# Performance work log

Hardware: AMD Instinct MI355X
Metric: run time of the kernel (lower is better)

Reference implementation:

```python
import jax, jax.numpy as jnp
import numpy as np

I = 256   # input_size
H = 256   # hidden_size
B = 64
T = 2048


def setup_inputs() -> dict:
    key = jax.random.key(0)
    ks = jax.random.split(key, 7)
    s_i = 1.0 / np.sqrt(I)
    s_h = 1.0 / np.sqrt(H)
    return {
        "x": jax.random.normal(ks[0], (B, T, I), dtype=jnp.float32),
        "h0": jax.random.normal(ks[1], (1, B, H), dtype=jnp.float32),
        "c0": jax.random.normal(ks[2], (1, B, H), dtype=jnp.float32),
        # Only l_fi / l_fh affect the output in the original forward (all four
        # gates are computed from the same pre-activation due to a source bug).
        "W_fi": jax.random.uniform(ks[3], (H, I), jnp.float32, -s_i, s_i),
        "b_fi": jax.random.uniform(ks[4], (H,), jnp.float32, -s_i, s_i),
        "W_fh": jax.random.uniform(ks[5], (H, H), jnp.float32, -s_h, s_h),
        "b_fh": jax.random.uniform(ks[6], (H,), jnp.float32, -s_h, s_h),
    }


def reference(x, h0, c0, W_fi, b_fi, W_fh, b_fh):
    # Faithful to the buggy torch source:
    #   f = i = o = sigmoid(l_fi(x_t) + l_fh(ht_1)); m = tanh(same)
    #   ht_1, ct_1 are NEVER updated -> no recurrence; vectorize over time.
    ht_1 = h0[0]  # (B, H), state[0].squeeze(0)
    ct_1 = c0[0]  # (B, H)
    gx = jnp.einsum('bti,hi->bth', x, W_fi) + b_fi          # (B, T, H)
    gh = ht_1 @ W_fh.T + b_fh                               # (B, H)
    g = gx + gh[:, None, :]                                 # (B, T, H)
    s = jax.nn.sigmoid(g)
    m = jnp.tanh(g)
    c = s * ct_1[:, None, :] + s * m                        # c_t per step
    h = s * jnp.tanh(c)                                     # h_t per step
    hidden_seq = jnp.transpose(h, (1, 0, 2))                # (T, B, H), cat dim=0
    return (hidden_seq, (h[:, -1, :], c[:, -1, :]))
```

## Files before the change

### kernel.cpp

```cpp
#include <hip/hip_runtime.h>
#include <hip/hip_bf16.h>
#include <stdint.h>

#define T_SZ 2048
#define B_SZ 64
#define H_SZ 256
#define I_SZ 256
#define M_SZ (B_SZ * T_SZ)
#define TBH  (T_SZ * B_SZ * H_SZ)

typedef float f32x4 __attribute__((ext_vector_type(4)));
typedef short s16x8 __attribute__((ext_vector_type(8)));

__device__ __forceinline__ unsigned pack_bf16(float a, float b) {
    unsigned ua = __float_as_uint(a);
    unsigned ub = __float_as_uint(b);
    ua += 0x7fffu + ((ua >> 16) & 1u);
    ub += 0x7fffu + ((ub >> 16) & 1u);
    return (ua >> 16) | (ub & 0xffff0000u);
}

__device__ __forceinline__ s16x8 pack8(float4 lo, float4 hi) {
    union { uint4 u; s16x8 v; } cv;
    cv.u.x = pack_bf16(lo.x, lo.y);
    cv.u.y = pack_bf16(lo.z, lo.w);
    cv.u.z = pack_bf16(hi.x, hi.y);
    cv.u.w = pack_bf16(hi.z, hi.w);
    return cv.v;
}

__device__ __forceinline__ void gload_lds16(const unsigned short* g, unsigned short* l) {
    __builtin_amdgcn_global_load_lds(
        (const __attribute__((address_space(1))) unsigned int*)g,
        (__attribute__((address_space(3))) unsigned int*)l,
        16, 0, 0);
}

__global__ void prep_kernel(const float* __restrict__ h0,
                            const float* __restrict__ W_fi,
                            const float* __restrict__ b_fi,
                            const float* __restrict__ W_fh,
                            const float* __restrict__ b_fh,
                            unsigned short* __restrict__ Wb,
                            float* __restrict__ gb) {
    __shared__ float h0s[H_SZ];
    const int b = blockIdx.x;
    const int h = threadIdx.x;
    h0s[h] = h0[b * H_SZ + h];
    __syncthreads();
    const float4* w4 = (const float4*)(W_fh + (size_t)h * H_SZ);
    float acc = 0.f;
#pragma unroll 16
    for (int j = 0; j < H_SZ / 4; ++j) {
        float4 w = w4[j];
        acc = fmaf(w.x, h0s[4 * j + 0], acc);
        acc = fmaf(w.y, h0s[4 * j + 1], acc);
        acc = fmaf(w.z, h0s[4 * j + 2], acc);
        acc = fmaf(w.w, h0s[4 * j + 3], acc);
    }
    gb[b * H_SZ + h] = acc + b_fi[h] + b_fh[h];

    const int e = (b * 256 + h) * 4;
    float4 wv = *(const float4*)(W_fi + e);
    uint2 pk;
    pk.x = pack_bf16(wv.x, wv.y);
    pk.y = pack_bf16(wv.z, wv.w);
    *(uint2*)(Wb + e) = pk;
}

__global__ __launch_bounds__(256, 4) void lstm_main(
    const float* __restrict__ x,
    const unsigned short* __restrict__ Wb,
    const float* __restrict__ gb,
    const float* __restrict__ c0,
    float* __restrict__ out) {
    __shared__ __align__(16) unsigned short Bs[64 * 256];

    const int tid  = threadIdx.x;
    const int lane = tid & 63;
    const int wid  = tid >> 6;
    const int bid  = blockIdx.x;
    const int n0 = (bid & 3) * 64;
    const int m0 = (bid >> 2) * 128;

#pragma unroll
    for (int i = 0; i < 8; ++i) {
        const int cbase = wid * 512 + i * 64;
        const int c = cbase + lane;
        const int row = c >> 5;
        const int kc = (lane & 31) ^ (row & 7);
        gload_lds16(Wb + (((size_t)(n0 + row)) << 8) + (kc << 3),
                    Bs + (size_t)cbase * 8);
    }

    const int fr = lane & 15, fq = lane >> 4;

    f32x4 acc[2][4];
#pragma unroll
    for (int mi = 0; mi < 2; ++mi)
#pragma unroll
        for (int ni = 0; ni < 4; ++ni)
            acc[mi][ni] = (f32x4){0.f, 0.f, 0.f, 0.f};

    const float* a0 = x + (size_t)(m0 + wid * 32 + fr) * I_SZ + fq * 8;
    const float* a1 = a0 + 16 * I_SZ;

    float4 p00 = *(const float4*)a0;
    float4 p01 = *(const float4*)(a0 + 4);
    float4 p10 = *(const float4*)a1;
    float4 p11 = *(const float4*)(a1 + 4);

    __syncthreads();

#pragma unroll
    for (int kt = 0; kt < 8; ++kt) {
        s16x8 af0 = pack8(p00, p01);
        s16x8 af1 = pack8(p10, p11);
        if (kt < 7) {
            const int ko = (kt + 1) * 32;
            p00 = *(const float4*)(a0 + ko);
            p01 = *(const float4*)(a0 + ko + 4);
            p10 = *(const float4*)(a1 + ko);
            p11 = *(const float4*)(a1 + ko + 4);
        }
        s16x8 bf[4];
#pragma unroll
        for (int ni = 0; ni < 4; ++ni) {
            const int nl = ni * 16 + fr;
            const int p = (kt * 4 + fq) ^ (nl & 7);
            bf[ni] = *(const s16x8*)(Bs + nl * 256 + p * 8);
        }
#pragma unroll
        for (int ni = 0; ni < 4; ++ni) {
            acc[0][ni] = __builtin_amdgcn_mfma_f32_16x16x32_bf16(af0, bf[ni], acc[0][ni], 0, 0, 0);
            acc[1][ni] = __builtin_amdgcn_mfma_f32_16x16x32_bf16(af1, bf[ni], acc[1][ni], 0, 0, 0);
        }
    }

    const int hbase = n0 + fr;
#pragma unroll
    for (int mi = 0; mi < 2; ++mi) {
#pragma unroll
        for (int r = 0; r < 4; ++r) {
            const int Mg = m0 + wid * 32 + mi * 16 + fq * 4 + r;
            const int bb = Mg >> 11;
            const int tt = Mg & (T_SZ - 1);
            float* orow = out + (size_t)tt * (B_SZ * H_SZ) + bb * H_SZ;
            const float* gbrow = gb + bb * H_SZ;
            const float* c0row = c0 + bb * H_SZ;
            const bool last = (tt == T_SZ - 1);
#pragma unroll
            for (int ni = 0; ni < 4; ++ni) {
                const int h = hbase + ni * 16;
                float g = acc[mi][ni][r] + gbrow[h];
                float e = __expf(-g);
                float s = __builtin_amdgcn_rcpf(1.f + e);
                float e2 = e * e;
                float m = (1.f - e2) * __builtin_amdgcn_rcpf(1.f + e2);
                float cv = s * (c0row[h] + m);
                float ec = __expf(-2.f * cv);
                float th = (1.f - ec) * __builtin_amdgcn_rcpf(1.f + ec);
                float hv = s * th;
                __builtin_nontemporal_store(hv, orow + h);
                if (last) {
                    out[TBH + bb * H_SZ + h] = hv;
                    out[TBH + B_SZ * H_SZ + bb * H_SZ + h] = cv;
                }
            }
        }
    }
}

extern "C" void kernel_launch(void* const* d_in, const int* in_sizes, int n_in,
                              void* d_out, int out_size, void* d_ws, size_t ws_size,
                              hipStream_t stream) {
    const float* x    = (const float*)d_in[0];
    const float* h0   = (const float*)d_in[1];
    const float* c0   = (const float*)d_in[2];
    const float* W_fi = (const float*)d_in[3];
    const float* b_fi = (const float*)d_in[4];
    const float* W_fh = (const float*)d_in[5];
    const float* b_fh = (const float*)d_in[6];
    float* out = (float*)d_out;

    unsigned short* Wb = (unsigned short*)d_ws;
    float* gb = (float*)((char*)d_ws + 131072);

    hipLaunchKernelGGL(prep_kernel, dim3(B_SZ), dim3(H_SZ), 0, stream,
                       h0, W_fi, b_fi, W_fh, b_fh, Wb, gb);
    hipLaunchKernelGGL(lstm_main, dim3(M_SZ / 128 * 4), dim3(256), 0, stream,
                       x, Wb, gb, c0, out);
}
```

Before: 303.7 us.

## Retile main kernel by timestep pairs for contiguous output writes

Each block now covers two timesteps across all 64 batches and half of H (128 columns), using 512 threads and a 128x256 bf16 weight tile in LDS. Rows are ordered by (batch, t), so each block writes a contiguous T-major output slab instead of scattering across timesteps as the old M=b*T+t tiling did. x reads, by contrast, become strided across batches. Each wave now computes a 16x128 tile with one A fragment per k-step, and the nontemporal store hint is dropped in favour of a plain store.

```diff
diff --git a/kernel.cpp b/kernel.cpp
--- a/kernel.cpp
+++ b/kernel.cpp
@@ -68,104 +68,90 @@
     *(uint2*)(Wb + e) = pk;
 }
 
-__global__ __launch_bounds__(256, 4) void lstm_main(
+__global__ __launch_bounds__(512, 4) void lstm_main(
     const float* __restrict__ x,
     const unsigned short* __restrict__ Wb,
     const float* __restrict__ gb,
     const float* __restrict__ c0,
     float* __restrict__ out) {
-    __shared__ __align__(16) unsigned short Bs[64 * 256];
+    __shared__ __align__(16) unsigned short Bs[128 * 256];
 
     const int tid  = threadIdx.x;
     const int lane = tid & 63;
     const int wid  = tid >> 6;
     const int bid  = blockIdx.x;
-    const int n0 = (bid & 3) * 64;
-    const int m0 = (bid >> 2) * 128;
+    const int n0  = (bid & 1) * 128;
+    const int tt0 = (bid >> 1) * 2;
 
 #pragma unroll
     for (int i = 0; i < 8; ++i) {
-        const int cbase = wid * 512 + i * 64;
-        const int c = cbase + lane;
-        const int row = c >> 5;
+        const int Pbase = (wid * 8 + i) * 64;
+        const int P = Pbase + lane;
+        const int row = P >> 5;
         const int kc = (lane & 31) ^ (row & 7);
-        gload_lds16(Wb + (((size_t)(n0 + row)) << 8) + (kc << 3),
-                    Bs + (size_t)cbase * 8);
+        gload_lds16(Wb + ((size_t)(n0 + row) << 8) + (kc << 3),
+                    Bs + (size_t)Pbase * 8);
     }
 
     const int fr = lane & 15, fq = lane >> 4;
 
-    f32x4 acc[2][4];
+    const int r = wid * 16 + fr;
+    const float* arow = x + ((size_t)((r >> 1) * T_SZ + tt0 + (r & 1)) << 8) + fq * 8;
+
+    f32x4 acc[8];
 #pragma unroll
-    for (int mi = 0; mi < 2; ++mi)
-#pragma unroll
-        for (int ni = 0; ni < 4; ++ni)
-            acc[mi][ni] = (f32x4){0.f, 0.f, 0.f, 0.f};
+    for (int ni = 0; ni < 8; ++ni) acc[ni] = (f32x4){0.f, 0.f, 0.f, 0.f};
 
-    const float* a0 = x + (size_t)(m0 + wid * 32 + fr) * I_SZ + fq * 8;
-    const float* a1 = a0 + 16 * I_SZ;
-
-    float4 p00 = *(const float4*)a0;
-    float4 p01 = *(const float4*)(a0 + 4);
-    float4 p10 = *(const float4*)a1;
-    float4 p11 = *(const float4*)(a1 + 4);
+    float4 u0[2], u1[2];
+    u0[0] = *(const float4*)(arow);      u1[0] = *(const float4*)(arow + 4);
+    u0[1] = *(const float4*)(arow + 32); u1[1] = *(const float4*)(arow + 36);
 
     __syncthreads();
 
 #pragma unroll
     for (int kt = 0; kt < 8; ++kt) {
-        s16x8 af0 = pack8(p00, p01);
-        s16x8 af1 = pack8(p10, p11);
-        if (kt < 7) {
-            const int ko = (kt + 1) * 32;
-            p00 = *(const float4*)(a0 + ko);
-            p01 = *(const float4*)(a0 + ko + 4);
-            p10 = *(const float4*)(a1 + ko);
-            p11 = *(const float4*)(a1 + ko + 4);
+        const s16x8 af = pack8(u0[kt & 1], u1[kt & 1]);
+        if (kt < 6) {
+            u0[kt & 1] = *(const float4*)(arow + (kt + 2) * 32);
+            u1[kt & 1] = *(const float4*)(arow + (kt + 2) * 32 + 4);
         }
-        s16x8 bf[4];
+        s16x8 bf[8];
 #pragma unroll
-        for (int ni = 0; ni < 4; ++ni) {
+        for (int ni = 0; ni < 8; ++ni) {
             const int nl = ni * 16 + fr;
             const int p = (kt * 4 + fq) ^ (nl & 7);
             bf[ni] = *(const s16x8*)(Bs + nl * 256 + p * 8);
         }
 #pragma unroll
-        for (int ni = 0; ni < 4; ++ni) {
-            acc[0][ni] = __builtin_amdgcn_mfma_f32_16x16x32_bf16(af0, bf[ni], acc[0][ni], 0, 0, 0);
-            acc[1][ni] = __builtin_amdgcn_mfma_f32_16x16x32_bf16(af1, bf[ni], acc[1][ni], 0, 0, 0);
-        }
+        for (int ni = 0; ni < 8; ++ni)
+            acc[ni] = __builtin_amdgcn_mfma_f32_16x16x32_bf16(af, bf[ni], acc[ni], 0, 0, 0);
     }
 
-    const int hbase = n0 + fr;
 #pragma unroll
-    for (int mi = 0; mi < 2; ++mi) {
+    for (int reg = 0; reg < 4; ++reg) {
+        const int rr = wid * 16 + fq * 4 + reg;
+        const int bb = rr >> 1;
+        const int tt = tt0 + (rr & 1);
+        float* orow = out + (size_t)tt * (B_SZ * H_SZ) + bb * H_SZ;
+        const float* gbrow = gb + bb * H_SZ;
+        const float* c0row = c0 + bb * H_SZ;
+        const bool last = (tt == T_SZ - 1);
 #pragma unroll
-        for (int r = 0; r < 4; ++r) {
-            const int Mg = m0 + wid * 32 + mi * 16 + fq * 4 + r;
-            const int bb = Mg >> 11;
-            const int tt = Mg & (T_SZ - 1);
-            float* orow = out + (size_t)tt * (B_SZ * H_SZ) + bb * H_SZ;
-            const float* gbrow = gb + bb * H_SZ;
-            const float* c0row = c0 + bb * H_SZ;
-            const bool last = (tt == T_SZ - 1);
-#pragma unroll
-            for (int ni = 0; ni < 4; ++ni) {
-                const int h = hbase + ni * 16;
-                float g = acc[mi][ni][r] + gbrow[h];
-                float e = __expf(-g);
-                float s = __builtin_amdgcn_rcpf(1.f + e);
-                float e2 = e * e;
-                float m = (1.f - e2) * __builtin_amdgcn_rcpf(1.f + e2);
-                float cv = s * (c0row[h] + m);
-                float ec = __expf(-2.f * cv);
-                float th = (1.f - ec) * __builtin_amdgcn_rcpf(1.f + ec);
-                float hv = s * th;
-                __builtin_nontemporal_store(hv, orow + h);
-                if (last) {
-                    out[TBH + bb * H_SZ + h] = hv;
-                    out[TBH + B_SZ * H_SZ + bb * H_SZ + h] = cv;
-                }
+        for (int ni = 0; ni < 8; ++ni) {
+            const int h = n0 + ni * 16 + fr;
+            float g = acc[ni][reg] + gbrow[h];
+            float e = __expf(-g);
+            float s = __builtin_amdgcn_rcpf(1.f + e);
+            float e2 = e * e;
+            float m = (1.f - e2) * __builtin_amdgcn_rcpf(1.f + e2);
+            float cv = s * (c0row[h] + m);
+            float ec = __expf(-2.f * cv);
+            float th = (1.f - ec) * __builtin_amdgcn_rcpf(1.f + ec);
+            float hv = s * th;
+            orow[h] = hv;
+            if (last) {
+                out[TBH + bb * H_SZ + h] = hv;
+                out[TBH + B_SZ * H_SZ + bb * H_SZ + h] = cv;
             }
         }
     }
@@ -188,6 +174,6 @@
 
     hipLaunchKernelGGL(prep_kernel, dim3(B_SZ), dim3(H_SZ), 0, stream,
                        h0, W_fi, b_fi, W_fh, b_fh, Wb, gb);
-    hipLaunchKernelGGL(lstm_main, dim3(M_SZ / 128 * 4), dim3(256), 0, stream,
+    hipLaunchKernelGGL(lstm_main, dim3(T_SZ), dim3(512), 0, stream,
                        x, Wb, gb, c0, out);
 }
```

Result: slower. 333.7 us (+9.9%).
